# Kernel tuning notes

Measured on AMD Instinct MI355X. Metric: run time of the kernel, lower is better.

The kernel has to match this reference:

```python
import jax, jax.numpy as jnp
import numpy as np

B, K = 128, 1024


def setup_inputs() -> dict:
    key = jax.random.key(0)
    k1, k2, k3, k4, k5 = jax.random.split(key, 5)
    scale = 1.0 / np.sqrt(K)  # torch Conv2d default init scale ~ 1/sqrt(fan_in)
    x = jax.random.normal(k1, (B, 1, K, K), dtype=jnp.float32)
    w_col = jax.random.uniform(k2, (K,), jnp.float32, -scale, scale)  # Conv2d(1,1,(1,K)) weight, squeezed
    b_col = jax.random.uniform(k3, (), jnp.float32, -scale, scale)
    w_row = jax.random.uniform(k4, (K,), jnp.float32, -scale, scale)  # Conv2d(1,1,(K,1)) weight, squeezed
    b_row = jax.random.uniform(k5, (), jnp.float32, -scale, scale)
    return {"x": x, "w_col": w_col, "b_col": b_col, "w_row": w_row, "b_row": b_row}


def reference(x, w_col, b_col, w_row, b_row):
    xs = x[:, 0]  # [B, K, K]
    # conv_column: kernel (1,K) -> contracts the width axis -> [B, K] (was [B,1,K,1])
    col = jnp.einsum('bij,j->bi', xs, w_col) + b_col
    # conv_row: kernel (K,1) -> contracts the height axis -> [B, K] (was [B,1,1,K])
    row = jnp.einsum('bij,i->bj', xs, w_row) + b_row
    # cat([conv_row]*K, dim=2): every row equals `row` -> [B, K, K]
    A = jnp.broadcast_to(row[:, None, :], (x.shape[0], K, K))
    # cat([conv_column]*K, dim=3): every column equals `col` -> [B, K, K]
    Bm = jnp.broadcast_to(col[:, :, None], (x.shape[0], K, K))
    out = jnp.matmul(A, Bm)  # [B, K, K]
    diag = jnp.diagonal(out, axis1=1, axis2=2)  # per-row torch.diag loop, vectorized
    return diag[:, None, :]  # [B, 1, K]
```

## Files before the change

kernel.cpp:

```cpp
#include <hip/hip_runtime.h>
#include <hip/hip_bf16.h>


#define K 1024
#define NB 128

typedef float f32x4 __attribute__((ext_vector_type(4)));

__global__ __launch_bounds__(256) void
rowcol_kernel(const float* __restrict__ x,
              const float* __restrict__ w_col,
              const float* __restrict__ w_row,
              float* __restrict__ col_ws,
              float* __restrict__ rowpart)
{
    const int bid  = blockIdx.x;
    const int b    = bid >> 4;
    const int rb   = bid & 15;
    const int row0 = rb * 64;
    const int tid  = threadIdx.x;
    const int wave = tid >> 6;
    const int lane = tid & 63;

    const float* xb = x + (size_t)b * K * K;

    const int rbu = __builtin_amdgcn_readfirstlane(row0 + wave * 16);

    f32x4 wc[4];
#pragma unroll
    for (int jt = 0; jt < 4; ++jt)
        wc[jt] = *reinterpret_cast<const f32x4*>(w_col + jt * 256 + lane * 4);

    f32x4 p[4];
#pragma unroll
    for (int jt = 0; jt < 4; ++jt) p[jt] = (f32x4){0.f, 0.f, 0.f, 0.f};

    float cacc[16];

    f32x4 buf[2][4];
    {
        const float* xr0 = xb + (size_t)rbu * K + lane * 4;
        const float* xr1 = xb + (size_t)(rbu + 1) * K + lane * 4;
#pragma unroll
        for (int jt = 0; jt < 4; ++jt)
            buf[0][jt] = __builtin_nontemporal_load(
                reinterpret_cast<const f32x4*>(xr0 + jt * 256));
#pragma unroll
        for (int jt = 0; jt < 4; ++jt)
            buf[1][jt] = __builtin_nontemporal_load(
                reinterpret_cast<const f32x4*>(xr1 + jt * 256));
    }

#pragma unroll
    for (int k = 0; k < 16; ++k) {
        f32x4 n0, n1, n2, n3;
        if (k < 14) {
            const float* xn = xb + (size_t)(rbu + k + 2) * K + lane * 4;
            n0 = __builtin_nontemporal_load(reinterpret_cast<const f32x4*>(xn +   0));
            n1 = __builtin_nontemporal_load(reinterpret_cast<const f32x4*>(xn + 256));
            n2 = __builtin_nontemporal_load(reinterpret_cast<const f32x4*>(xn + 512));
            n3 = __builtin_nontemporal_load(reinterpret_cast<const f32x4*>(xn + 768));
        }
        const float wr = w_row[rbu + k];
        f32x4 a0 = buf[k & 1][0], a1 = buf[k & 1][1];
        f32x4 a2 = buf[k & 1][2], a3 = buf[k & 1][3];
        f32x4 c4;
        c4  = a0 * wc[0];
        c4 += a1 * wc[1];
        c4 += a2 * wc[2];
        c4 += a3 * wc[3];
        p[0] += a0 * wr;
        p[1] += a1 * wr;
        p[2] += a2 * wr;
        p[3] += a3 * wr;
        cacc[k] = (c4.x + c4.y) + (c4.z + c4.w);
        if (k < 14) {
            buf[k & 1][0] = n0; buf[k & 1][1] = n1;
            buf[k & 1][2] = n2; buf[k & 1][3] = n3;
        }
    }

#pragma unroll
    for (int lvl = 0; lvl < 4; ++lvl) {
        const int s = 1 << lvl;
        const int n = 16 >> (lvl + 1);
#pragma unroll
        for (int m = 0; m < n; ++m) {
            float a  = cacc[2 * m]     + __shfl_xor(cacc[2 * m],     s);
            float bb = cacc[2 * m + 1] + __shfl_xor(cacc[2 * m + 1], s);
            cacc[m] = (lane & s) ? bb : a;
        }
    }
    float r = cacc[0];
    r += __shfl_xor(r, 16);
    r += __shfl_xor(r, 32);
    if (lane < 16) col_ws[b * K + rbu + lane] = r;

    __shared__ float rp[4][K];
#pragma unroll
    for (int jt = 0; jt < 4; ++jt)
        *reinterpret_cast<f32x4*>(&rp[wave][jt * 256 + lane * 4]) = p[jt];
    __syncthreads();

    const int j0 = tid * 4;
    f32x4 s0 = *reinterpret_cast<const f32x4*>(&rp[0][j0]);
    f32x4 s1 = *reinterpret_cast<const f32x4*>(&rp[1][j0]);
    f32x4 s2 = *reinterpret_cast<const f32x4*>(&rp[2][j0]);
    f32x4 s3 = *reinterpret_cast<const f32x4*>(&rp[3][j0]);
    f32x4 s = (s0 + s1) + (s2 + s3);
    *reinterpret_cast<f32x4*>(&rowpart[(size_t)bid * K + j0]) = s;
}

__global__ __launch_bounds__(256) void
finalize_kernel(const float* __restrict__ col_ws,
                const float* __restrict__ rowpart,
                const float* __restrict__ b_col_p,
                const float* __restrict__ b_row_p,
                float* __restrict__ out)
{
    const int b    = blockIdx.x;
    const int tid  = threadIdx.x;
    const int wave = tid >> 6;
    const int lane = tid & 63;
    const float bc = b_col_p[0];
    const float br = b_row_p[0];

    const int j0 = tid * 4;
    f32x4 c = *reinterpret_cast<const f32x4*>(&col_ws[b * K + j0]);
    f32x4 r = (f32x4){0.f, 0.f, 0.f, 0.f};
#pragma unroll
    for (int pblk = 0; pblk < 16; ++pblk)
        r += *reinterpret_cast<const f32x4*>(
            &rowpart[((size_t)(b * 16 + pblk)) * K + j0]);

    float acc = (c.x + bc) * (r.x + br)
              + (c.y + bc) * (r.y + br)
              + (c.z + bc) * (r.z + br)
              + (c.w + bc) * (r.w + br);
#pragma unroll
    for (int off = 32; off; off >>= 1) acc += __shfl_xor(acc, off);

    __shared__ float red[4];
    if (lane == 0) red[wave] = acc;
    __syncthreads();
    const float S = red[0] + red[1] + red[2] + red[3];

    f32x4 o = (f32x4){S, S, S, S};
    *reinterpret_cast<f32x4*>(&out[b * K + j0]) = o;
}

extern "C" void kernel_launch(void* const* d_in, const int* in_sizes, int n_in,
                              void* d_out, int out_size, void* d_ws, size_t ws_size,
                              hipStream_t stream) {
    const float* x     = (const float*)d_in[0];
    const float* w_col = (const float*)d_in[1];
    const float* b_col = (const float*)d_in[2];
    const float* w_row = (const float*)d_in[3];
    const float* b_row = (const float*)d_in[4];
    float* out = (float*)d_out;

    float* col_ws  = (float*)d_ws;
    float* rowpart = col_ws + (size_t)NB * K;

    rowcol_kernel<<<NB * 16, 256, 0, stream>>>(x, w_col, w_row, col_ws, rowpart);
    finalize_kernel<<<NB, 256, 0, stream>>>(col_ws, rowpart, b_col, b_row, out);
}
```

Measured before the change: 99.22 us.

## Fuse finalize into main kernel via last-block atomic counter per batch

Merges the two-kernel pipeline into one kernel: each block publishes its column and row partials with relaxed agent-scope atomic stores, then increments a per-batch counter. The sixteenth block to finish for a batch does an acquire fence and performs the final reduction and output write. This removes the second kernel launch and the gap between kernels, but adds a memset of the counters and scalarised atomic stores for the row partials.

Measured after the change: 121.4 us. +22.3%, slower.

```diff
diff --git a/kernel.cpp b/kernel.cpp
--- a/kernel.cpp
+++ b/kernel.cpp
@@ -8,11 +8,15 @@
 typedef float f32x4 __attribute__((ext_vector_type(4)));
 
 __global__ __launch_bounds__(256) void
-rowcol_kernel(const float* __restrict__ x,
-              const float* __restrict__ w_col,
-              const float* __restrict__ w_row,
-              float* __restrict__ col_ws,
-              float* __restrict__ rowpart)
+fused_kernel(const float* __restrict__ x,
+             const float* __restrict__ w_col,
+             const float* __restrict__ w_row,
+             const float* __restrict__ b_col_p,
+             const float* __restrict__ b_row_p,
+             float* __restrict__ out,
+             float* __restrict__ col_ws,
+             float* __restrict__ rowpart,
+             int* __restrict__ counters)
 {
     const int bid  = blockIdx.x;
     const int b    = bid >> 4;
@@ -94,7 +98,9 @@
     float r = cacc[0];
     r += __shfl_xor(r, 16);
     r += __shfl_xor(r, 32);
-    if (lane < 16) col_ws[b * K + rbu + lane] = r;
+    if (lane < 16)
+        __hip_atomic_store(&col_ws[b * K + rbu + lane], r,
+                           __ATOMIC_RELAXED, __HIP_MEMORY_SCOPE_AGENT);
 
     __shared__ float rp[4][K];
 #pragma unroll
@@ -103,40 +109,42 @@
     __syncthreads();
 
     const int j0 = tid * 4;
-    f32x4 s0 = *reinterpret_cast<const f32x4*>(&rp[0][j0]);
-    f32x4 s1 = *reinterpret_cast<const f32x4*>(&rp[1][j0]);
-    f32x4 s2 = *reinterpret_cast<const f32x4*>(&rp[2][j0]);
-    f32x4 s3 = *reinterpret_cast<const f32x4*>(&rp[3][j0]);
-    f32x4 s = (s0 + s1) + (s2 + s3);
-    *reinterpret_cast<f32x4*>(&rowpart[(size_t)bid * K + j0]) = s;
-}
+    {
+        f32x4 s0 = *reinterpret_cast<const f32x4*>(&rp[0][j0]);
+        f32x4 s1 = *reinterpret_cast<const f32x4*>(&rp[1][j0]);
+        f32x4 s2 = *reinterpret_cast<const f32x4*>(&rp[2][j0]);
+        f32x4 s3 = *reinterpret_cast<const f32x4*>(&rp[3][j0]);
+        f32x4 s = (s0 + s1) + (s2 + s3);
+        float* dst = &rowpart[(size_t)bid * K + j0];
+        __hip_atomic_store(dst + 0, s.x, __ATOMIC_RELAXED, __HIP_MEMORY_SCOPE_AGENT);
+        __hip_atomic_store(dst + 1, s.y, __ATOMIC_RELAXED, __HIP_MEMORY_SCOPE_AGENT);
+        __hip_atomic_store(dst + 2, s.z, __ATOMIC_RELAXED, __HIP_MEMORY_SCOPE_AGENT);
+        __hip_atomic_store(dst + 3, s.w, __ATOMIC_RELAXED, __HIP_MEMORY_SCOPE_AGENT);
+    }
 
-__global__ __launch_bounds__(256) void
-finalize_kernel(const float* __restrict__ col_ws,
-                const float* __restrict__ rowpart,
-                const float* __restrict__ b_col_p,
-                const float* __restrict__ b_row_p,
-                float* __restrict__ out)
-{
-    const int b    = blockIdx.x;
-    const int tid  = threadIdx.x;
-    const int wave = tid >> 6;
-    const int lane = tid & 63;
+    __syncthreads();
+    __shared__ int sprev;
+    if (tid == 0)
+        sprev = __hip_atomic_fetch_add(&counters[b], 1,
+                                       __ATOMIC_RELAXED, __HIP_MEMORY_SCOPE_AGENT);
+    __syncthreads();
+    if (sprev != 15) return;
+
+    __builtin_amdgcn_fence(__ATOMIC_ACQUIRE, "agent");
+
+    f32x4 c = *reinterpret_cast<const f32x4*>(&col_ws[b * K + j0]);
+    f32x4 rsum = (f32x4){0.f, 0.f, 0.f, 0.f};
+#pragma unroll
+    for (int pblk = 0; pblk < 16; ++pblk)
+        rsum += *reinterpret_cast<const f32x4*>(
+            &rowpart[((size_t)(b * 16 + pblk)) * K + j0]);
+
     const float bc = b_col_p[0];
     const float br = b_row_p[0];
-
-    const int j0 = tid * 4;
-    f32x4 c = *reinterpret_cast<const f32x4*>(&col_ws[b * K + j0]);
-    f32x4 r = (f32x4){0.f, 0.f, 0.f, 0.f};
-#pragma unroll
-    for (int pblk = 0; pblk < 16; ++pblk)
-        r += *reinterpret_cast<const f32x4*>(
-            &rowpart[((size_t)(b * 16 + pblk)) * K + j0]);
-
-    float acc = (c.x + bc) * (r.x + br)
-              + (c.y + bc) * (r.y + br)
-              + (c.z + bc) * (r.z + br)
-              + (c.w + bc) * (r.w + br);
+    float acc = (c.x + bc) * (rsum.x + br)
+              + (c.y + bc) * (rsum.y + br)
+              + (c.z + bc) * (rsum.z + br)
+              + (c.w + bc) * (rsum.w + br);
 #pragma unroll
     for (int off = 32; off; off >>= 1) acc += __shfl_xor(acc, off);
 
@@ -159,9 +167,11 @@
     const float* b_row = (const float*)d_in[4];
     float* out = (float*)d_out;
 
-    float* col_ws  = (float*)d_ws;
-    float* rowpart = col_ws + (size_t)NB * K;
+    float* col_ws   = (float*)d_ws;
+    float* rowpart  = col_ws + (size_t)NB * K;
+    int*   counters = (int*)(rowpart + (size_t)NB * 16 * K);
 
-    rowcol_kernel<<<NB * 16, 256, 0, stream>>>(x, w_col, w_row, col_ws, rowpart);
-    finalize_kernel<<<NB, 256, 0, stream>>>(col_ws, rowpart, b_col, b_row, out);
+    hipMemsetAsync(counters, 0, NB * sizeof(int), stream);
+    fused_kernel<<<NB * 16, 256, 0, stream>>>(x, w_col, w_row, b_col, b_row,
+                                              out, col_ws, rowpart, counters);
 }
```
